# Kernel optimization log

Hardware: AMD Instinct MI355X
Metric: run time of the kernel (lower is better)

## Reference

```python
import jax, jax.numpy as jnp
import numpy as np

B, T, D, H, R = 4, 4096, 1024, 16, 256
DH = D // H  # 64


def setup_inputs() -> dict:
    key = jax.random.key(0)
    ks = jax.random.split(key, 5)
    s = 0.02
    return {
        "x": jax.random.normal(ks[0], (B, T, D), dtype=jnp.float32),
        "Wq": jax.random.normal(ks[1], (D, D), dtype=jnp.float32) * s,
        "bq": jnp.zeros((D,), dtype=jnp.float32),
        "Wd": jax.random.normal(ks[2], (D, R), dtype=jnp.float32) * s,
        "bd": jnp.zeros((R,), dtype=jnp.float32),
        "Wu": jax.random.normal(ks[3], (R, 2 * D), dtype=jnp.float32) * s,
        "bu": jnp.zeros((2 * D,), dtype=jnp.float32),
        "Wo": jax.random.normal(ks[4], (D, D), dtype=jnp.float32) * s,
        "bo": jnp.zeros((D,), dtype=jnp.float32),
    }


def reference(x, Wq, bq, Wd, bd, Wu, bu, Wo, bo):
    b, t = x.shape[0], x.shape[1]
    # q projection -> (B,T,H,DH)
    q = (x @ Wq + bq).reshape(b, t, H, DH)
    # low-rank KV: down then up -> (B,T,H,2*DH)
    kv = ((x @ Wd + bd) @ Wu + bu).reshape(b, t, H, 2 * DH)
    k, v = kv[..., :DH], kv[..., DH:]
    # elu+1 feature map
    q = jax.nn.elu(q) + 1.0
    k = jax.nn.elu(k) + 1.0
    # linear attention: context = k^T v per head -> (B,H,DH,DH)
    context = jnp.einsum("bthd,bthe->bhde", k, v)
    out = jnp.einsum("bthd,bhde->bthe", q, context)  # (B,T,H,DH)
    # normalizer: q . sum_t(k)
    k_sum = k.sum(axis=1)  # (B,H,DH)
    z = 1.0 / (jnp.einsum("bthd,bhd->bth", q, k_sum) + 1e-6)
    out = out * z[..., None]
    return out.reshape(b, t, D) @ Wo + bo
```

## Files before the change

kernel.cpp:

```cpp
#include <hip/hip_runtime.h>
#include <hip/hip_bf16.h>
#include <cstddef>
#include <cstdint>

#define B_  4
#define T_  4096
#define D_  1024
#define H_  16
#define DH_ 64
#define R_  256
#define BT_ (B_ * T_)
#define TWO_D_ (2 * D_)

typedef __attribute__((ext_vector_type(8))) short short8;
typedef __attribute__((ext_vector_type(4))) float f32x4;

__device__ __forceinline__ float elu1(float x) {
    return x > 0.0f ? x + 1.0f : __expf(x);
}

__device__ __forceinline__ float bf2f(short u) {
    union { uint32_t i; float f; } c;
    c.i = ((uint32_t)(uint16_t)u) << 16;
    return c.f;
}

typedef __attribute__((address_space(1))) void void_g;
typedef __attribute__((address_space(3))) void void_l;
__device__ __forceinline__ void gld_lds16(const void* g, void* l) {
    __builtin_amdgcn_global_load_lds(
        (const void_g*)(uintptr_t)g,
        (void_l*)(uint32_t)(uintptr_t)l,
        16, 0, 0);
}

#define BM 128
#define BN 128
#define BK 32

__device__ __forceinline__ void store_out(float* p, float v) { *p = v; }
__device__ __forceinline__ void store_out(__hip_bfloat16* p, float v) { *p = __float2bfloat16(v); }

template<int EPI, bool BROW, typename OT>
__global__ __launch_bounds__(256) void gemm_bf16(
    const __hip_bfloat16* __restrict__ A,
    const __hip_bfloat16* __restrict__ Bt,
    const float* __restrict__ bias,
    OT* __restrict__ C,
    OT* __restrict__ C2,
    int M, int N, int K)
{
    __shared__ alignas(16) __hip_bfloat16 As[BM * BK];
    __shared__ alignas(16) __hip_bfloat16 Bs[BN * BK];

    const int nbx = N / BN;
    const int id = blockIdx.x;
    const int strip = id / (8 * nbx);
    const int wi = id % (8 * nbx);
    const int bm = (strip * 8 + (wi & 7)) * BM;
    const int bn = (wi >> 3) * BN;

    const int tid  = threadIdx.x;
    const int lane = tid & 63;
    const int wm   = (tid >> 7) * 64;
    const int wn   = ((tid >> 6) & 1) * 64;
    const int r15  = lane & 15;
    const int kg   = lane >> 4;

    f32x4 acc[4][4] = {};

    const int c0 = tid, c1 = tid + 256;
    const __hip_bfloat16* a0 = A  + (size_t)(bm + (c0 >> 2)) * K + (c0 & 3) * 8;
    const __hip_bfloat16* a1 = A  + (size_t)(bm + (c1 >> 2)) * K + (c1 & 3) * 8;
    const __hip_bfloat16* b0 = Bt + (size_t)(bn + (c0 >> 2)) * K + (c0 & 3) * 8;
    const __hip_bfloat16* b1 = Bt + (size_t)(bn + (c1 >> 2)) * K + (c1 & 3) * 8;

    for (int k0 = 0; k0 < K; k0 += BK) {
        gld_lds16(a0 + k0, As + c0 * 8);
        gld_lds16(a1 + k0, As + c1 * 8);
        gld_lds16(b0 + k0, Bs + c0 * 8);
        gld_lds16(b1 + k0, Bs + c1 * 8);
        __syncthreads();

        short8 af[4], bf[4];
#pragma unroll
        for (int i = 0; i < 4; ++i) {
            af[i] = *(const short8*)(As + (wm + i * 16 + r15) * BK + kg * 8);
            bf[i] = *(const short8*)(Bs + (wn + i * 16 + r15) * BK + kg * 8);
        }
#pragma unroll
        for (int i = 0; i < 4; ++i)
#pragma unroll
            for (int j = 0; j < 4; ++j)
                acc[i][j] = __builtin_amdgcn_mfma_f32_16x16x32_bf16(af[i], bf[j], acc[i][j], 0, 0, 0);
        __syncthreads();
    }

    const int row0 = bm + wm + (lane >> 4) * 4;

    if (EPI == 3) {
        const bool qreg = (bn < 1024);
#pragma unroll
        for (int j = 0; j < 4; ++j) {
            const int col = bn + wn + j * 16 + r15;
            const float bv = bias[col];
#pragma unroll
            for (int i = 0; i < 4; ++i)
#pragma unroll
                for (int r = 0; r < 4; ++r) {
                    const int row = row0 + i * 16 + r;
                    float v = acc[i][j][r] + bv;
                    if (qreg) {
                        store_out(C + (size_t)row * 1024 + col, elu1(v));
                    } else {
                        store_out(C2 + (size_t)row * 256 + (col - 1024), v);
                    }
                }
        }
        return;
    }

    float brow[4][4];
    if (BROW) {
#pragma unroll
        for (int i = 0; i < 4; ++i)
#pragma unroll
            for (int r = 0; r < 4; ++r) brow[i][r] = bias[row0 + i * 16 + r];
    }
#pragma unroll
    for (int j = 0; j < 4; ++j) {
        const int col = bn + wn + j * 16 + r15;
        const float bv = BROW ? 0.0f : bias[col];
        const bool kp_col = ((col & 127) < 64);
#pragma unroll
        for (int i = 0; i < 4; ++i) {
#pragma unroll
            for (int r = 0; r < 4; ++r) {
                const int row = row0 + i * 16 + r;
                float v = acc[i][j][r] + (BROW ? brow[i][r] : bv);
                if (EPI == 1) v = elu1(v);
                else if (EPI == 2) {
                    const bool kp = BROW ? ((row & 127) < 64) : kp_col;
                    if (kp) v = elu1(v);
                }
                store_out(C + (size_t)row * N + col, v);
            }
        }
    }
}

__global__ __launch_bounds__(256) void cast_bf16_kernel(
    const float* __restrict__ s, __hip_bfloat16* __restrict__ d, int n)
{
    const int i = (blockIdx.x * 256 + threadIdx.x) * 8;
    if (i >= n) return;
    float4 v0 = *(const float4*)(s + i);
    float4 v1 = *(const float4*)(s + i + 4);
    __hip_bfloat16 t[8];
    t[0] = __float2bfloat16(v0.x); t[1] = __float2bfloat16(v0.y);
    t[2] = __float2bfloat16(v0.z); t[3] = __float2bfloat16(v0.w);
    t[4] = __float2bfloat16(v1.x); t[5] = __float2bfloat16(v1.y);
    t[6] = __float2bfloat16(v1.z); t[7] = __float2bfloat16(v1.w);
    *(short8*)(d + i) = *(const short8*)t;
}

__global__ __launch_bounds__(256) void transpose_cast(
    const float* __restrict__ W, __hip_bfloat16* __restrict__ Wt, int K, int N)
{
    __shared__ float t[32][33];
    const int n0 = blockIdx.x * 32, k0 = blockIdx.y * 32;
    const int c = threadIdx.x & 31, r = threadIdx.x >> 5;
#pragma unroll
    for (int rr = r; rr < 32; rr += 8)
        t[rr][c] = W[(size_t)(k0 + rr) * N + n0 + c];
    __syncthreads();
#pragma unroll
    for (int rr = r; rr < 32; rr += 8)
        Wt[(size_t)(n0 + rr) * K + k0 + c] = __float2bfloat16(t[c][rr]);
}

__global__ __launch_bounds__(256) void concat_bias(
    const float* __restrict__ bq, const float* __restrict__ bd,
    float* __restrict__ o)
{
    const int i = blockIdx.x * 256 + threadIdx.x;
    o[i] = (i < 1024) ? bq[i] : bd[i - 1024];
}

#define CHT 512

__global__ __launch_bounds__(256) void ctx_mfma(
    const __hip_bfloat16* __restrict__ kvT, float* __restrict__ ctx,
    float* __restrict__ ksum)
{
    __shared__ alignas(16) unsigned char smem[40960];
    float* red0 = (float*)smem;
    float* red1 = (float*)(smem + 20480);

    const int bh = blockIdx.x >> 3;
    const int chunk = blockIdx.x & 7;
    const int b = bh >> 4;
    const int h = bh & 15;
    const int tid = threadIdx.x;
    const int lane = tid & 63;
    const int w = tid >> 6;
    const int r15 = lane & 15;
    const int kg  = lane >> 4;

    f32x4 acc[4][4] = {};
    f32x4 acc4[4] = {};

    const short one = (short)0x3F80;
    const short8 bfv = (r15 == 0)
        ? (short8){one, one, one, one, one, one, one, one}
        : (short8){0, 0, 0, 0, 0, 0, 0, 0};

    const size_t tbase = (size_t)b * T_ + (size_t)chunk * CHT;
    const __hip_bfloat16* src = kvT + (size_t)(h * 128) * BT_ + tbase;

    for (int it = 0; it < CHT / 128; ++it) {
#pragma unroll
        for (int r = 0; r < 8; ++r) {
            const int c = r * 256 + tid;
            const int s = c >> 9, j = (c >> 2) & 127, u = c & 3;
            gld_lds16(src + (size_t)j * BT_ + it * 128 + s * 32 + u * 8,
                      smem + c * 16);
        }
        __syncthreads();

        const __hip_bfloat16* Ls = (const __hip_bfloat16*)smem;
        short8 af[4], bf[4];
#pragma unroll
        for (int i = 0; i < 4; ++i) {
            af[i] = *(const short8*)(Ls + (w * 128 + i * 16 + r15) * 32 + kg * 8);
            bf[i] = *(const short8*)(Ls + (w * 128 + 64 + i * 16 + r15) * 32 + kg * 8);
        }
#pragma unroll
        for (int i = 0; i < 4; ++i) {
#pragma unroll
            for (int j = 0; j < 4; ++j)
                acc[i][j] = __builtin_amdgcn_mfma_f32_16x16x32_bf16(af[i], bf[j], acc[i][j], 0, 0, 0);
            acc4[i] = __builtin_amdgcn_mfma_f32_16x16x32_bf16(af[i], bfv, acc4[i], 0, 0, 0);
        }
        __syncthreads();
    }

    const int q4 = lane >> 4;
    auto wr = [&](float* reg) {
#pragma unroll
        for (int i = 0; i < 4; ++i) {
#pragma unroll
            for (int r = 0; r < 4; ++r) {
                const int row = i * 16 + q4 * 4 + r;
#pragma unroll
                for (int j = 0; j < 4; ++j) reg[row * 80 + j * 16 + r15] = acc[i][j][r];
                reg[row * 80 + 64 + r15] = acc4[i][r];
            }
        }
    };
    auto rd = [&](const float* reg) {
#pragma unroll
        for (int i = 0; i < 4; ++i) {
#pragma unroll
            for (int r = 0; r < 4; ++r) {
                const int row = i * 16 + q4 * 4 + r;
#pragma unroll
                for (int j = 0; j < 4; ++j) acc[i][j][r] += reg[row * 80 + j * 16 + r15];
                acc4[i][r] += reg[row * 80 + 64 + r15];
            }
        }
    };

    if (w == 1) wr(red0);
    if (w == 3) wr(red1);
    __syncthreads();
    if (w == 0) rd(red0);
    if (w == 2) rd(red1);
    __syncthreads();
    if (w == 2) wr(red0);
    __syncthreads();
    if (w == 0) { rd(red0); wr(red0); }
    __syncthreads();

    float* cdst = ctx + (size_t)bh * 4096;
#pragma unroll
    for (int r = 0; r < 16; ++r) {
        const int idx = r * 256 + tid;
        const int d = idx >> 6, e = idx & 63;
        atomicAdd(cdst + idx, red0[d * 80 + e]);
    }
    if (tid < 64) atomicAdd(ksum + bh * 64 + tid, red0[tid * 80 + 64]);
}

__global__ __launch_bounds__(256) void pack_ctx(
    const float* __restrict__ ctx, __hip_bfloat16* __restrict__ ctxT)
{
    __shared__ float L[64 * 65];
    const int bh = blockIdx.x;
    const int tid = threadIdx.x;
#pragma unroll
    for (int r = 0; r < 16; ++r) {
        const int idx = r * 256 + tid;
        L[(idx >> 6) * 65 + (idx & 63)] = ctx[(size_t)bh * 4096 + idx];
    }
    __syncthreads();
#pragma unroll
    for (int r = 0; r < 16; ++r) {
        const int idx = r * 256 + tid;
        ctxT[(size_t)bh * 4096 + idx] =
            __float2bfloat16(L[(idx & 63) * 65 + (idx >> 6)]);
    }
}

__global__ __launch_bounds__(256) void out_mfma(
    const __hip_bfloat16* __restrict__ qb, const __hip_bfloat16* __restrict__ ctxT,
    const float* __restrict__ ksum, __hip_bfloat16* __restrict__ outb)
{
    __shared__ alignas(16) unsigned char As[256 * 128];
    __shared__ alignas(16) unsigned char Bs[64 * 128];
    __shared__ float ksumL[64];
    __shared__ float zbuf[256];

    const int bh = blockIdx.x >> 4;
    const int tile = blockIdx.x & 15;
    const int b = bh >> 4;
    const int h = bh & 15;
    const int tid = threadIdx.x;
    const int lane = tid & 63;
    const int w = tid >> 6;
    const int r15 = lane & 15;
    const int kg  = lane >> 4;

    const size_t trow0 = (size_t)b * T_ + (size_t)tile * 256;

#pragma unroll
    for (int r = 0; r < 8; ++r) {
        const int c = r * 256 + tid;
        const int row = c >> 3, slot = c & 7, u = slot ^ (row & 7);
        gld_lds16(qb + (trow0 + row) * D_ + h * 64 + u * 8, As + c * 16);
    }
#pragma unroll
    for (int r = 0; r < 2; ++r) {
        const int c = r * 256 + tid;
        const int row = c >> 3, slot = c & 7, u = slot ^ (row & 7);
        gld_lds16(ctxT + (size_t)bh * 4096 + row * 64 + u * 8, Bs + c * 16);
    }
    if (tid < 64) ksumL[tid] = ksum[bh * 64 + tid];
    __syncthreads();

    short8 af[4][2], bf[4][2];
#pragma unroll
    for (int i = 0; i < 4; ++i)
#pragma unroll
        for (int s = 0; s < 2; ++s) {
            const int m = w * 64 + i * 16 + r15;
            const int n = i * 16 + r15;
            const int uk = s * 4 + kg;
            af[i][s] = *(const short8*)(As + m * 128 + ((uk ^ (m & 7)) * 16));
            bf[i][s] = *(const short8*)(Bs + n * 128 + ((uk ^ (n & 7)) * 16));
        }

    f32x4 acc[4][4] = {};
#pragma unroll
    for (int s = 0; s < 2; ++s)
#pragma unroll
        for (int i = 0; i < 4; ++i)
#pragma unroll
            for (int j = 0; j < 4; ++j)
                acc[i][j] = __builtin_amdgcn_mfma_f32_16x16x32_bf16(af[i][s], bf[j][s], acc[i][j], 0, 0, 0);

    float dsum[4];
#pragma unroll
    for (int i = 0; i < 4; ++i) {
        float s0 = 0.0f;
#pragma unroll
        for (int s = 0; s < 2; ++s)
#pragma unroll
            for (int j8 = 0; j8 < 8; ++j8)
                s0 += bf2f(af[i][s][j8]) * ksumL[s * 32 + kg * 8 + j8];
        s0 += __shfl_xor(s0, 16);
        s0 += __shfl_xor(s0, 32);
        dsum[i] = s0;
    }
    if (lane < 16) {
#pragma unroll
        for (int i = 0; i < 4; ++i)
            zbuf[w * 64 + i * 16 + lane] = 1.0f / (dsum[i] + 1e-6f);
    }
    __syncthreads();

    const int q4 = lane >> 4;
#pragma unroll
    for (int i = 0; i < 4; ++i) {
#pragma unroll
        for (int r = 0; r < 4; ++r) {
            const int m = w * 64 + i * 16 + q4 * 4 + r;
            const float z = zbuf[m];
#pragma unroll
            for (int j = 0; j < 4; ++j) {
                outb[(trow0 + m) * D_ + h * 64 + j * 16 + r15] =
                    __float2bfloat16(acc[i][j][r] * z);
            }
        }
    }
}

extern "C" void kernel_launch(void* const* d_in, const int* in_sizes, int n_in,
                              void* d_out, int out_size, void* d_ws, size_t ws_size,
                              hipStream_t stream) {
    const float* x  = (const float*)d_in[0];
    const float* Wq = (const float*)d_in[1];
    const float* bq = (const float*)d_in[2];
    const float* Wd = (const float*)d_in[3];
    const float* bd = (const float*)d_in[4];
    const float* Wu = (const float*)d_in[5];
    const float* bu = (const float*)d_in[6];
    const float* Wo = (const float*)d_in[7];
    const float* bo = (const float*)d_in[8];
    float* out = (float*)d_out;

    __hip_bfloat16* xb    = (__hip_bfloat16*)d_ws;
    __hip_bfloat16* WqdT  = xb    + (size_t)BT_ * D_;
    __hip_bfloat16* WuT   = WqdT  + (size_t)1280 * D_;
    __hip_bfloat16* WoT   = WuT   + (size_t)TWO_D_ * R_;
    __hip_bfloat16* xdb   = WoT   + (size_t)D_ * D_;
    __hip_bfloat16* kvT   = xdb   + (size_t)BT_ * R_;
    __hip_bfloat16* qb    = kvT   + (size_t)TWO_D_ * BT_;
    float* bias_qd = (float*)(qb + (size_t)BT_ * D_);
    float* ctx  = bias_qd + 1280;
    float* ksum = ctx + (size_t)B_ * H_ * DH_ * DH_;
    __hip_bfloat16* ctxT = (__hip_bfloat16*)(ksum + B_ * H_ * DH_);
    __hip_bfloat16* outb = xb;

    hipMemsetAsync(ctx, 0,
        (size_t)(B_ * H_ * DH_ * DH_ + B_ * H_ * DH_) * sizeof(float), stream);

    cast_bf16_kernel<<<(BT_ * D_) / (8 * 256), 256, 0, stream>>>(x, xb, BT_ * D_);
    transpose_cast<<<dim3(D_ / 32, D_ / 32), 256, 0, stream>>>(Wq, WqdT, D_, D_);
    transpose_cast<<<dim3(R_ / 32, D_ / 32), 256, 0, stream>>>(Wd, WqdT + (size_t)D_ * D_, D_, R_);
    transpose_cast<<<dim3(TWO_D_ / 32, R_ / 32), 256, 0, stream>>>(Wu, WuT, R_, TWO_D_);
    transpose_cast<<<dim3(D_ / 32, D_ / 32), 256, 0, stream>>>(Wo, WoT, D_, D_);
    concat_bias<<<5, 256, 0, stream>>>(bq, bd, bias_qd);

    gemm_bf16<3, false, __hip_bfloat16><<<(BT_ / BM) * (1280 / BN), 256, 0, stream>>>(
        xb, WqdT, bias_qd, qb, xdb, BT_, 1280, D_);
    gemm_bf16<2, true, __hip_bfloat16><<<(TWO_D_ / BM) * (BT_ / BN), 256, 0, stream>>>(
        WuT, xdb, bu, kvT, nullptr, TWO_D_, BT_, R_);
    ctx_mfma<<<64 * (T_ / CHT), 256, 0, stream>>>(kvT, ctx, ksum);
    pack_ctx<<<64, 256, 0, stream>>>(ctx, ctxT);
    out_mfma<<<64 * 16, 256, 0, stream>>>(qb, ctxT, ksum, outb);
    gemm_bf16<0, false, float><<<(BT_ / BM) * (D_ / BN), 256, 0, stream>>>(
        outb, WoT, bo, out, nullptr, BT_, D_, D_);
}
```

Before: 353.8 us.

## Multi-buffer GEMM LDS tiles with prefetch depth three and vmcnt waits

Turns the single-buffered GEMM K loop into a 5-deep LDS ring: three stages are prefetched with global_load_lds, and each iteration issues the load three tiles ahead before waiting with a counted vmcnt and a barrier. The trailing __syncthreads is dropped, since the ring spacing keeps a slot from being overwritten while it is still being read. The aim is to hide global load latency behind the MFMA work. In exchange LDS use grows to 80KB per block, which may lower occupancy, and the hand-written vmcnt counts rely on exactly four loads per stage.

```diff
diff --git a/kernel.cpp b/kernel.cpp
--- a/kernel.cpp
+++ b/kernel.cpp
@@ -37,6 +37,7 @@
 #define BM 128
 #define BN 128
 #define BK 32
+#define NBUF 5
 
 __device__ __forceinline__ void store_out(float* p, float v) { *p = v; }
 __device__ __forceinline__ void store_out(__hip_bfloat16* p, float v) { *p = __float2bfloat16(v); }
@@ -50,8 +51,8 @@
     OT* __restrict__ C2,
     int M, int N, int K)
 {
-    __shared__ alignas(16) __hip_bfloat16 As[BM * BK];
-    __shared__ alignas(16) __hip_bfloat16 Bs[BN * BK];
+    __shared__ alignas(16) __hip_bfloat16 As[NBUF * BM * BK];
+    __shared__ alignas(16) __hip_bfloat16 Bs[NBUF * BN * BK];
 
     const int nbx = N / BN;
     const int id = blockIdx.x;
@@ -75,25 +76,47 @@
     const __hip_bfloat16* b0 = Bt + (size_t)(bn + (c0 >> 2)) * K + (c0 & 3) * 8;
     const __hip_bfloat16* b1 = Bt + (size_t)(bn + (c1 >> 2)) * K + (c1 & 3) * 8;
 
-    for (int k0 = 0; k0 < K; k0 += BK) {
-        gld_lds16(a0 + k0, As + c0 * 8);
-        gld_lds16(a1 + k0, As + c1 * 8);
-        gld_lds16(b0 + k0, Bs + c0 * 8);
-        gld_lds16(b1 + k0, Bs + c1 * 8);
-        __syncthreads();
+    const int nk = K / BK;
+
+    auto stage = [&](int t) {
+        const int buf = t % NBUF;
+        __hip_bfloat16* Ad = As + buf * (BM * BK);
+        __hip_bfloat16* Bd = Bs + buf * (BN * BK);
+        const int k0 = t * BK;
+        gld_lds16(a0 + k0, Ad + c0 * 8);
+        gld_lds16(a1 + k0, Ad + c1 * 8);
+        gld_lds16(b0 + k0, Bd + c0 * 8);
+        gld_lds16(b1 + k0, Bd + c1 * 8);
+    };
+
+    stage(0); stage(1); stage(2);
+
+    for (int t = 0; t < nk; ++t) {
+        if (t + 3 < nk) {
+            stage(t + 3);
+            asm volatile("s_waitcnt vmcnt(12)\ns_barrier" ::: "memory");
+        } else if (t + 2 < nk) {
+            asm volatile("s_waitcnt vmcnt(8)\ns_barrier" ::: "memory");
+        } else if (t + 1 < nk) {
+            asm volatile("s_waitcnt vmcnt(4)\ns_barrier" ::: "memory");
+        } else {
+            asm volatile("s_waitcnt vmcnt(0)\ns_barrier" ::: "memory");
+        }
+
+        const __hip_bfloat16* Asb = As + (t % NBUF) * (BM * BK);
+        const __hip_bfloat16* Bsb = Bs + (t % NBUF) * (BN * BK);
 
         short8 af[4], bf[4];
 #pragma unroll
         for (int i = 0; i < 4; ++i) {
-            af[i] = *(const short8*)(As + (wm + i * 16 + r15) * BK + kg * 8);
-            bf[i] = *(const short8*)(Bs + (wn + i * 16 + r15) * BK + kg * 8);
+            af[i] = *(const short8*)(Asb + (wm + i * 16 + r15) * BK + kg * 8);
+            bf[i] = *(const short8*)(Bsb + (wn + i * 16 + r15) * BK + kg * 8);
         }
 #pragma unroll
         for (int i = 0; i < 4; ++i)
 #pragma unroll
             for (int j = 0; j < 4; ++j)
                 acc[i][j] = __builtin_amdgcn_mfma_f32_16x16x32_bf16(af[i], bf[j], acc[i][j], 0, 0, 0);
-        __syncthreads();
     }
 
     const int row0 = bm + wm + (lane >> 4) * 4;
```

New measurement: 335.3 us. 5.2% less time.
